# Kernel tuning notes

Hardware: AMD Instinct MI355X
Metric: run time of the kernel (lower is better)

The kernel has to match this reference:

```python
import jax, jax.numpy as jnp
import numpy as np

B, S, D, H = 4, 2048, 1024, 16
HD = D // H  # per-head dim = 64


def setup_inputs() -> dict:
    key = jax.random.key(0)
    ks = jax.random.split(key, 9)
    s = 1.0 / np.sqrt(HD)
    return {
        "query": jax.random.normal(ks[0], (B, S, D), jnp.float32),
        "key_": jax.random.normal(ks[1], (B, S, D), jnp.float32),
        "value": jax.random.normal(ks[2], (B, S, D), jnp.float32),
        "Wq": jax.random.uniform(ks[3], (HD, HD), jnp.float32, -s, s),
        "bq": jax.random.uniform(ks[4], (HD,), jnp.float32, -s, s),
        "Wk": jax.random.uniform(ks[5], (HD, HD), jnp.float32, -s, s),
        "bk": jax.random.uniform(ks[6], (HD,), jnp.float32, -s, s),
        "Wv": jax.random.uniform(ks[7], (HD, HD), jnp.float32, -s, s),
        "bv": jax.random.uniform(ks[8], (HD,), jnp.float32, -s, s),
    }


def _split_heads(x):
    # [B,S,D] -> [B,H,S,hd]
    return x.reshape(B, S, H, HD).transpose(0, 2, 1, 3)


def reference(query, key_, value, Wq, bq, Wk, bk, Wv, bv):
    q = _split_heads(query) @ Wq.T + bq  # [B,H,S,hd]
    k = _split_heads(key_) @ Wk.T + bk
    v = _split_heads(value) @ Wv.T + bv
    scores = jnp.einsum("bhqd,bhkd->bhqk", q, k) / jnp.sqrt(jnp.float32(HD))
    weights = jax.nn.softmax(scores, axis=-1)
    x_att = jnp.einsum("bhqk,bhkd->bhqd", weights, v)  # [B,H,S,hd]
    return x_att.transpose(0, 2, 1, 3).reshape(B, S, D)
```

## Files before the change

kernel.cpp:

```cpp
#include <hip/hip_runtime.h>
#include <hip/hip_bf16.h>


typedef float f32x4 __attribute__((ext_vector_type(4)));
typedef float f32x16 __attribute__((ext_vector_type(16)));
typedef __bf16 bf16x8 __attribute__((ext_vector_type(8)));
typedef unsigned short u16x4 __attribute__((ext_vector_type(4)));
typedef unsigned int u32x4 __attribute__((ext_vector_type(4)));

#define S_LEN 2048
#define D_MODEL 1024
#define HDIM 64
#define BH_TOT 64

static __device__ __forceinline__ unsigned short f2bf(float x) {
    __bf16 h = (__bf16)x;
    return __builtin_bit_cast(unsigned short, h);
}
static __device__ __forceinline__ unsigned int pk2(float lo, float hi) {
    return (unsigned int)f2bf(lo) | ((unsigned int)f2bf(hi) << 16);
}
static __device__ __forceinline__ bf16x8 cvt8(f32x4 a, f32x4 b) {
    bf16x8 r;
    #pragma unroll
    for (int j = 0; j < 4; ++j) { r[j] = (__bf16)a[j]; r[4 + j] = (__bf16)b[j]; }
    return r;
}

__global__ __launch_bounds__(256) void proj_kernel(
    const float* __restrict__ qin, const float* __restrict__ kin, const float* __restrict__ vin,
    const float* __restrict__ Wq, const float* __restrict__ bq,
    const float* __restrict__ Wk, const float* __restrict__ bk,
    const float* __restrict__ Wv, const float* __restrict__ bv,
    unsigned short* __restrict__ ws)
{
    const int bid = blockIdx.x;
    const int mat = bid >> 11;
    const int rem = bid & 2047;
    const int bh  = rem >> 5;
    const int st  = rem & 31;
    const int b = bh >> 4, h = bh & 15;

    const int tid = threadIdx.x;
    const int wave = tid >> 6, l = tid & 63;
    const int lr = l & 15, lg = l >> 4;

    const float* X    = (mat == 0) ? qin : (mat == 1) ? kin : vin;
    const float* W    = (mat == 0) ? Wq  : (mat == 1) ? Wk  : Wv;
    const float* bias = (mat == 0) ? bq  : (mat == 1) ? bk  : bv;

    const int s0 = st * 64 + wave * 16;

    bf16x8 af[2];
    {
        const size_t rowoff = ((size_t)(b * S_LEN + s0 + lr)) * D_MODEL + h * HDIM + lg * 8;
        #pragma unroll
        for (int kk = 0; kk < 2; ++kk) {
            const f32x4* p = (const f32x4*)(X + rowoff + kk * 32);
            af[kk] = cvt8(p[0], p[1]);
        }
    }
    bf16x8 wf[4][2];
    #pragma unroll
    for (int nt = 0; nt < 4; ++nt)
        #pragma unroll
        for (int kk = 0; kk < 2; ++kk) {
            const f32x4* p = (const f32x4*)(W + (nt * 16 + lr) * HDIM + kk * 32 + lg * 8);
            wf[nt][kk] = cvt8(p[0], p[1]);
        }

    unsigned short* qws  = ws;
    unsigned short* kws  = ws + (size_t)BH_TOT * S_LEN * HDIM;
    unsigned short* vtws = ws + 2 * (size_t)BH_TOT * S_LEN * HDIM;

    if (mat < 2) {
        f32x4 acc[4];
        #pragma unroll
        for (int nt = 0; nt < 4; ++nt)
            acc[nt] = *(const f32x4*)(bias + nt * 16 + lg * 4);
        #pragma unroll
        for (int nt = 0; nt < 4; ++nt)
            #pragma unroll
            for (int kk = 0; kk < 2; ++kk)
                acc[nt] = __builtin_amdgcn_mfma_f32_16x16x32_bf16(wf[nt][kk], af[kk], acc[nt], 0, 0, 0);

        const float sc = (mat == 0) ? 0.18033688011112042f : 1.0f;
        unsigned short* dst = (mat == 0) ? qws : kws;
        const size_t rowbase = ((size_t)bh * S_LEN + s0 + lr) * HDIM;
        #pragma unroll
        for (int nt = 0; nt < 4; ++nt) {
            u16x4 u;
            #pragma unroll
            for (int r = 0; r < 4; ++r) u[r] = f2bf(acc[nt][r] * sc);
            *(u16x4*)(dst + rowbase + nt * 16 + lg * 4) = u;
        }
    } else {
        f32x4 acc[4];
        #pragma unroll
        for (int nt = 0; nt < 4; ++nt) {
            float bb = bias[nt * 16 + lr];
            acc[nt][0] = bb; acc[nt][1] = bb; acc[nt][2] = bb; acc[nt][3] = bb;
        }
        #pragma unroll
        for (int nt = 0; nt < 4; ++nt)
            #pragma unroll
            for (int kk = 0; kk < 2; ++kk)
                acc[nt] = __builtin_amdgcn_mfma_f32_16x16x32_bf16(af[kk], wf[nt][kk], acc[nt], 0, 0, 0);
        #pragma unroll
        for (int nt = 0; nt < 4; ++nt) {
            u16x4 u;
            #pragma unroll
            for (int r = 0; r < 4; ++r) u[r] = f2bf(acc[nt][r]);
            *(u16x4*)(vtws + ((size_t)bh * HDIM + nt * 16 + lr) * S_LEN + s0 + lg * 4) = u;
        }
    }
}

__global__ __launch_bounds__(256, 3) void attn_kernel(
    const unsigned short* __restrict__ ws, float* __restrict__ out)
{
    const unsigned short* qws  = ws;
    const unsigned short* kws  = ws + (size_t)BH_TOT * S_LEN * HDIM;
    const unsigned short* vtws = ws + 2 * (size_t)BH_TOT * S_LEN * HDIM;

    __shared__ u32x4 ldsbuf[1024];
    char* ldsK = (char*)ldsbuf;
    char* ldsV = (char*)ldsbuf + 8192;

    const int bid = blockIdx.x;
    const int qt = bid & 15, bh = bid >> 4;
    const int b = bh >> 4, h = bh & 15;
    const int tid = threadIdx.x, wave = tid >> 6, l = tid & 63;
    const int q32 = l & 31, hi = l >> 5;

    const int qrow = qt * 128 + wave * 32 + q32;
    bf16x8 qf[4];
    {
        const unsigned short* qp = qws + ((size_t)bh * S_LEN + qrow) * HDIM + hi * 8;
        #pragma unroll
        for (int s = 0; s < 4; ++s) qf[s] = *(const bf16x8*)(qp + s * 16);
    }

    float m_run = -1e30f, l_run = 0.f;
    f32x16 oacc[2];
    #pragma unroll
    for (int i = 0; i < 16; ++i) { oacc[0][i] = 0.f; oacc[1][i] = 0.f; }

    const int srow = tid >> 3;
    const int scol = (tid & 7) * 16;
    const unsigned short* kbase = kws + (size_t)bh * S_LEN * HDIM;
    const unsigned short* vbase = vtws + (size_t)bh * HDIM * S_LEN;

    for (int t = 0; t < S_LEN / 64; ++t) {
        const int kv0 = t * 64;
        __syncthreads();
        #pragma unroll
        for (int p = 0; p < 2; ++p) {
            const int r = srow + p * 32;
            u32x4 val = *(const u32x4*)((const char*)(kbase + (size_t)(kv0 + r) * HDIM) + scol);
            *(u32x4*)(&ldsK[r * 128 + (scol ^ ((r & 7) << 4))]) = val;
        }
        #pragma unroll
        for (int p = 0; p < 2; ++p) {
            const int d = srow + p * 32;
            u32x4 val = *(const u32x4*)((const char*)(vbase + (size_t)d * S_LEN + kv0) + scol);
            *(u32x4*)(&ldsV[d * 128 + (scol ^ ((d & 7) << 4))]) = val;
        }
        __syncthreads();

        f32x16 sacc[2];
        #pragma unroll
        for (int i = 0; i < 16; ++i) { sacc[0][i] = 0.f; sacc[1][i] = 0.f; }
        #pragma unroll
        for (int m = 0; m < 2; ++m) {
            const int row = m * 32 + q32;
            const int swz = (row & 7) << 4;
            #pragma unroll
            for (int s = 0; s < 4; ++s) {
                bf16x8 kf = *(const bf16x8*)(&ldsK[row * 128 + ((s * 32 + hi * 16) ^ swz)]);
                sacc[m] = __builtin_amdgcn_mfma_f32_32x32x16_bf16(kf, qf[s], sacc[m], 0, 0, 0);
            }
        }

        float mx0 = sacc[0][0], mx1 = sacc[0][1], mx2 = sacc[0][2], mx3 = sacc[0][3];
        #pragma unroll
        for (int i = 4; i < 16; i += 4) {
            mx0 = fmaxf(mx0, sacc[0][i + 0]); mx1 = fmaxf(mx1, sacc[0][i + 1]);
            mx2 = fmaxf(mx2, sacc[0][i + 2]); mx3 = fmaxf(mx3, sacc[0][i + 3]);
        }
        #pragma unroll
        for (int i = 0; i < 16; i += 4) {
            mx0 = fmaxf(mx0, sacc[1][i + 0]); mx1 = fmaxf(mx1, sacc[1][i + 1]);
            mx2 = fmaxf(mx2, sacc[1][i + 2]); mx3 = fmaxf(mx3, sacc[1][i + 3]);
        }
        float pmax = fmaxf(fmaxf(mx0, mx1), fmaxf(mx2, mx3));
        pmax = fmaxf(pmax, __shfl_xor(pmax, 32));

        if (!__all(pmax <= m_run + 8.0f)) {
            const float mnew = fmaxf(m_run, pmax);
            const float fs = exp2f(m_run - mnew);
            m_run = mnew;
            l_run *= fs;
            #pragma unroll
            for (int reg = 0; reg < 16; ++reg) {
                const int qrw = (reg & 3) + 8 * (reg >> 2) + 4 * hi;
                const float fr = __shfl(fs, qrw);
                oacc[0][reg] *= fr; oacc[1][reg] *= fr;
            }
        }

        float s0a = 0.f, s1a = 0.f, s2a = 0.f, s3a = 0.f;
        #pragma unroll
        for (int m = 0; m < 2; ++m)
            #pragma unroll
            for (int i = 0; i < 16; i += 4) {
                float e0 = exp2f(sacc[m][i + 0] - m_run);
                float e1 = exp2f(sacc[m][i + 1] - m_run);
                float e2 = exp2f(sacc[m][i + 2] - m_run);
                float e3 = exp2f(sacc[m][i + 3] - m_run);
                sacc[m][i + 0] = e0; sacc[m][i + 1] = e1;
                sacc[m][i + 2] = e2; sacc[m][i + 3] = e3;
                s0a += e0; s1a += e1; s2a += e2; s3a += e3;
            }
        float rsum = (s0a + s1a) + (s2a + s3a);
        l_run += rsum + __shfl_xor(rsum, 32);

        bf16x8 pa[4];
        #pragma unroll
        for (int s = 0; s < 4; ++s) {
            const int m = s >> 1, rb = (s & 1) * 8;
            unsigned int c0 = pk2(sacc[m][rb + 0], sacc[m][rb + 1]);
            unsigned int c1 = pk2(sacc[m][rb + 2], sacc[m][rb + 3]);
            unsigned int c2 = pk2(sacc[m][rb + 4], sacc[m][rb + 5]);
            unsigned int c3 = pk2(sacc[m][rb + 6], sacc[m][rb + 7]);
            asm("v_permlane32_swap_b32 %0, %1" : "+v"(c0), "+v"(c2));
            asm("v_permlane32_swap_b32 %0, %1" : "+v"(c1), "+v"(c3));
            u32x4 packed = { c0, c1, c2, c3 };
            pa[s] = __builtin_bit_cast(bf16x8, packed);
        }

        #pragma unroll
        for (int dcol = 0; dcol < 2; ++dcol) {
            const int row = dcol * 32 + q32;
            const int swz = (row & 7) << 4;
            #pragma unroll
            for (int s = 0; s < 4; ++s) {
                bf16x8 vf = *(const bf16x8*)(&ldsV[row * 128 + ((s * 32 + hi * 16) ^ swz)]);
                oacc[dcol] = __builtin_amdgcn_mfma_f32_32x32x16_bf16(pa[s], vf, oacc[dcol], 0, 0, 0);
            }
        }
    }

    const float linv = 1.0f / l_run;
    float* obase = out + ((size_t)(b * S_LEN + qt * 128 + wave * 32)) * D_MODEL + h * HDIM;
    #pragma unroll
    for (int reg = 0; reg < 16; ++reg) {
        const int qrw = (reg & 3) + 8 * (reg >> 2) + 4 * hi;
        const float li = __shfl(linv, qrw);
        float* po = obase + (size_t)qrw * D_MODEL + q32;
        po[0]  = oacc[0][reg] * li;
        po[32] = oacc[1][reg] * li;
    }
}

extern "C" void kernel_launch(void* const* d_in, const int* in_sizes, int n_in,
                              void* d_out, int out_size, void* d_ws, size_t ws_size,
                              hipStream_t stream) {
    const float* qin = (const float*)d_in[0];
    const float* kin = (const float*)d_in[1];
    const float* vin = (const float*)d_in[2];
    const float* Wq  = (const float*)d_in[3];
    const float* bq  = (const float*)d_in[4];
    const float* Wk  = (const float*)d_in[5];
    const float* bk  = (const float*)d_in[6];
    const float* Wv  = (const float*)d_in[7];
    const float* bv  = (const float*)d_in[8];
    unsigned short* ws = (unsigned short*)d_ws;
    float* out = (float*)d_out;

    proj_kernel<<<dim3(3 * 2048), dim3(256), 0, stream>>>(qin, kin, vin, Wq, bq, Wk, bk, Wv, bv, ws);
    attn_kernel<<<dim3(1024), dim3(256), 0, stream>>>(ws, out);
}
```

Baseline: 312.5 us.

## Double-buffer K/V via direct global-to-LDS loads, split V projection with LDS transpose

The attention kernel now stages K and V tiles into double-buffered LDS using global_load_lds, prefetching the next tile while computing the current one. It also raises wave priority around the MFMA blocks and remaps block indices so heads group per XCD for L2 locality. The V projection moves into its own kernel that transposes through LDS so the transposed V is written with wide coalesced stores. The costs are twice the LDS per block, which may reduce occupancy, and one extra kernel launch.

```diff
diff --git a/kernel.cpp b/kernel.cpp
--- a/kernel.cpp
+++ b/kernel.cpp
@@ -26,12 +26,15 @@
     for (int j = 0; j < 4; ++j) { r[j] = (__bf16)a[j]; r[4 + j] = (__bf16)b[j]; }
     return r;
 }
-
-__global__ __launch_bounds__(256) void proj_kernel(
-    const float* __restrict__ qin, const float* __restrict__ kin, const float* __restrict__ vin,
+static __device__ __forceinline__ void gl_lds16(const void* g, void* l) {
+    __builtin_amdgcn_global_load_lds((const __attribute__((address_space(1))) void*)g,
+                                     (__attribute__((address_space(3))) void*)l, 16, 0, 0);
+}
+
+__global__ __launch_bounds__(256) void projqk_kernel(
+    const float* __restrict__ qin, const float* __restrict__ kin,
     const float* __restrict__ Wq, const float* __restrict__ bq,
     const float* __restrict__ Wk, const float* __restrict__ bk,
-    const float* __restrict__ Wv, const float* __restrict__ bv,
     unsigned short* __restrict__ ws)
 {
     const int bid = blockIdx.x;
@@ -45,9 +48,9 @@
     const int wave = tid >> 6, l = tid & 63;
     const int lr = l & 15, lg = l >> 4;
 
-    const float* X    = (mat == 0) ? qin : (mat == 1) ? kin : vin;
-    const float* W    = (mat == 0) ? Wq  : (mat == 1) ? Wk  : Wv;
-    const float* bias = (mat == 0) ? bq  : (mat == 1) ? bk  : bv;
+    const float* X    = (mat == 0) ? qin : kin;
+    const float* W    = (mat == 0) ? Wq  : Wk;
+    const float* bias = (mat == 0) ? bq  : bk;
 
     const int s0 = st * 64 + wave * 16;
 
@@ -69,51 +72,93 @@
             wf[nt][kk] = cvt8(p[0], p[1]);
         }
 
-    unsigned short* qws  = ws;
-    unsigned short* kws  = ws + (size_t)BH_TOT * S_LEN * HDIM;
+    f32x4 acc[4];
+    #pragma unroll
+    for (int nt = 0; nt < 4; ++nt)
+        acc[nt] = *(const f32x4*)(bias + nt * 16 + lg * 4);
+    #pragma unroll
+    for (int nt = 0; nt < 4; ++nt)
+        #pragma unroll
+        for (int kk = 0; kk < 2; ++kk)
+            acc[nt] = __builtin_amdgcn_mfma_f32_16x16x32_bf16(wf[nt][kk], af[kk], acc[nt], 0, 0, 0);
+
+    unsigned short* qws = ws;
+    unsigned short* kws = ws + (size_t)BH_TOT * S_LEN * HDIM;
+    const float sc = (mat == 0) ? 0.18033688011112042f : 1.0f;
+    unsigned short* dst = (mat == 0) ? qws : kws;
+    const size_t rowbase = ((size_t)bh * S_LEN + s0 + lr) * HDIM;
+    #pragma unroll
+    for (int nt = 0; nt < 4; ++nt) {
+        u16x4 u;
+        #pragma unroll
+        for (int r = 0; r < 4; ++r) u[r] = f2bf(acc[nt][r] * sc);
+        *(u16x4*)(dst + rowbase + nt * 16 + lg * 4) = u;
+    }
+}
+
+__global__ __launch_bounds__(256) void projv_kernel(
+    const float* __restrict__ vin,
+    const float* __restrict__ Wv, const float* __restrict__ bv,
+    unsigned short* __restrict__ ws)
+{
+    const int bid = blockIdx.x;
+    const int bh  = bid >> 5;
+    const int st  = bid & 31;
+    const int b = bh >> 4, h = bh & 15;
+
+    const int tid = threadIdx.x;
+    const int wave = tid >> 6, l = tid & 63;
+    const int lr = l & 15, lg = l >> 4;
+
+    __shared__ unsigned short T[64][72];
+
+    const int s0 = st * 64 + wave * 16;
+
+    bf16x8 af[2];
+    {
+        const size_t rowoff = ((size_t)(b * S_LEN + s0 + lr)) * D_MODEL + h * HDIM + lg * 8;
+        #pragma unroll
+        for (int kk = 0; kk < 2; ++kk) {
+            const f32x4* p = (const f32x4*)(vin + rowoff + kk * 32);
+            af[kk] = cvt8(p[0], p[1]);
+        }
+    }
+    bf16x8 wf[4][2];
+    #pragma unroll
+    for (int nt = 0; nt < 4; ++nt)
+        #pragma unroll
+        for (int kk = 0; kk < 2; ++kk) {
+            const f32x4* p = (const f32x4*)(Wv + (nt * 16 + lr) * HDIM + kk * 32 + lg * 8);
+            wf[nt][kk] = cvt8(p[0], p[1]);
+        }
+
+    f32x4 acc[4];
+    #pragma unroll
+    for (int nt = 0; nt < 4; ++nt) {
+        float bb = bv[nt * 16 + lr];
+        acc[nt][0] = bb; acc[nt][1] = bb; acc[nt][2] = bb; acc[nt][3] = bb;
+    }
+    #pragma unroll
+    for (int nt = 0; nt < 4; ++nt)
+        #pragma unroll
+        for (int kk = 0; kk < 2; ++kk)
+            acc[nt] = __builtin_amdgcn_mfma_f32_16x16x32_bf16(af[kk], wf[nt][kk], acc[nt], 0, 0, 0);
+
+    #pragma unroll
+    for (int nt = 0; nt < 4; ++nt) {
+        u16x4 u;
+        #pragma unroll
+        for (int r = 0; r < 4; ++r) u[r] = f2bf(acc[nt][r]);
+        *(u16x4*)&T[nt * 16 + lr][wave * 16 + lg * 4] = u;
+    }
+    __syncthreads();
+
     unsigned short* vtws = ws + 2 * (size_t)BH_TOT * S_LEN * HDIM;
-
-    if (mat < 2) {
-        f32x4 acc[4];
-        #pragma unroll
-        for (int nt = 0; nt < 4; ++nt)
-            acc[nt] = *(const f32x4*)(bias + nt * 16 + lg * 4);
-        #pragma unroll
-        for (int nt = 0; nt < 4; ++nt)
-            #pragma unroll
-            for (int kk = 0; kk < 2; ++kk)
-                acc[nt] = __builtin_amdgcn_mfma_f32_16x16x32_bf16(wf[nt][kk], af[kk], acc[nt], 0, 0, 0);
-
-        const float sc = (mat == 0) ? 0.18033688011112042f : 1.0f;
-        unsigned short* dst = (mat == 0) ? qws : kws;
-        const size_t rowbase = ((size_t)bh * S_LEN + s0 + lr) * HDIM;
-        #pragma unroll
-        for (int nt = 0; nt < 4; ++nt) {
-            u16x4 u;
-            #pragma unroll
-            for (int r = 0; r < 4; ++r) u[r] = f2bf(acc[nt][r] * sc);
-            *(u16x4*)(dst + rowbase + nt * 16 + lg * 4) = u;
-        }
-    } else {
-        f32x4 acc[4];
-        #pragma unroll
-        for (int nt = 0; nt < 4; ++nt) {
-            float bb = bias[nt * 16 + lr];
-            acc[nt][0] = bb; acc[nt][1] = bb; acc[nt][2] = bb; acc[nt][3] = bb;
-        }
-        #pragma unroll
-        for (int nt = 0; nt < 4; ++nt)
-            #pragma unroll
-            for (int kk = 0; kk < 2; ++kk)
-                acc[nt] = __builtin_amdgcn_mfma_f32_16x16x32_bf16(af[kk], wf[nt][kk], acc[nt], 0, 0, 0);
-        #pragma unroll
-        for (int nt = 0; nt < 4; ++nt) {
-            u16x4 u;
-            #pragma unroll
-            for (int r = 0; r < 4; ++r) u[r] = f2bf(acc[nt][r]);
-            *(u16x4*)(vtws + ((size_t)bh * HDIM + nt * 16 + lr) * S_LEN + s0 + lg * 4) = u;
-        }
-    }
+    const int d = tid >> 2, sc = (tid & 3) * 16;
+    const uint4* srcp = (const uint4*)&T[d][sc];
+    unsigned short* dstp = vtws + ((size_t)bh * HDIM + d) * S_LEN + st * 64 + sc;
+    ((uint4*)dstp)[0] = srcp[0];
+    ((uint4*)dstp)[1] = srcp[1];
 }
 
 __global__ __launch_bounds__(256, 3) void attn_kernel(
@@ -123,13 +168,15 @@
     const unsigned short* kws  = ws + (size_t)BH_TOT * S_LEN * HDIM;
     const unsigned short* vtws = ws + 2 * (size_t)BH_TOT * S_LEN * HDIM;
 
-    __shared__ u32x4 ldsbuf[1024];
-    char* ldsK = (char*)ldsbuf;
-    char* ldsV = (char*)ldsbuf + 8192;
+    __shared__ u32x4 ldsraw[2048];
+    char* ldsbuf = (char*)ldsraw;
 
     const int bid = blockIdx.x;
-    const int qt = bid & 15, bh = bid >> 4;
+    const int xcd = bid & 7, idx = bid >> 3;
+    const int qt = idx & 15;
+    const int bh = xcd + ((idx >> 4) << 3);
     const int b = bh >> 4, h = bh & 15;
+
     const int tid = threadIdx.x, wave = tid >> 6, l = tid & 63;
     const int q32 = l & 31, hi = l >> 5;
 
@@ -146,31 +193,44 @@
     #pragma unroll
     for (int i = 0; i < 16; ++i) { oacc[0][i] = 0.f; oacc[1][i] = 0.f; }
 
-    const int srow = tid >> 3;
-    const int scol = (tid & 7) * 16;
-    const unsigned short* kbase = kws + (size_t)bh * S_LEN * HDIM;
-    const unsigned short* vbase = vtws + (size_t)bh * HDIM * S_LEN;
+    const int lrow  = l >> 3;
+    const int lswz  = ((l & 7) * 16) ^ (lrow << 4);
+    const char* kgb = (const char*)(kws + (size_t)bh * S_LEN * HDIM);
+    const char* vgb = (const char*)(vtws + (size_t)bh * HDIM * S_LEN);
+
+    #define STAGE(bsel, kv0)                                                        \
+        do {                                                                        \
+            char* bK_ = ldsbuf + (bsel) * 16384;                                    \
+            char* bV_ = bK_ + 8192;                                                 \
+            _Pragma("unroll")                                                       \
+            for (int i_ = 0; i_ < 2; ++i_) {                                        \
+                const int r_ = wave * 16 + i_ * 8 + lrow;                           \
+                gl_lds16(kgb + (size_t)((kv0) + r_) * 128 + lswz,                   \
+                         bK_ + wave * 2048 + i_ * 1024);                            \
+                gl_lds16(vgb + (size_t)r_ * (S_LEN * 2) + (kv0) * 2 + lswz,         \
+                         bV_ + wave * 2048 + i_ * 1024);                            \
+            }                                                                       \
+        } while (0)
+
+    STAGE(0, 0);
+    int cur = 0;
 
     for (int t = 0; t < S_LEN / 64; ++t) {
-        const int kv0 = t * 64;
-        __syncthreads();
-        #pragma unroll
-        for (int p = 0; p < 2; ++p) {
-            const int r = srow + p * 32;
-            u32x4 val = *(const u32x4*)((const char*)(kbase + (size_t)(kv0 + r) * HDIM) + scol);
-            *(u32x4*)(&ldsK[r * 128 + (scol ^ ((r & 7) << 4))]) = val;
-        }
-        #pragma unroll
-        for (int p = 0; p < 2; ++p) {
-            const int d = srow + p * 32;
-            u32x4 val = *(const u32x4*)((const char*)(vbase + (size_t)d * S_LEN + kv0) + scol);
-            *(u32x4*)(&ldsV[d * 128 + (scol ^ ((d & 7) << 4))]) = val;
-        }
-        __syncthreads();
+        if (t < S_LEN / 64 - 1) {
+            STAGE(cur ^ 1, (t + 1) * 64);
+            asm volatile("s_waitcnt vmcnt(4)" ::: "memory");
+        } else {
+            asm volatile("s_waitcnt vmcnt(0)" ::: "memory");
+        }
+        __builtin_amdgcn_s_barrier();
+
+        const char* ldsK = ldsbuf + cur * 16384;
+        const char* ldsV = ldsK + 8192;
 
         f32x16 sacc[2];
         #pragma unroll
         for (int i = 0; i < 16; ++i) { sacc[0][i] = 0.f; sacc[1][i] = 0.f; }
+        __builtin_amdgcn_s_setprio(1);
         #pragma unroll
         for (int m = 0; m < 2; ++m) {
             const int row = m * 32 + q32;
@@ -181,6 +241,7 @@
                 sacc[m] = __builtin_amdgcn_mfma_f32_32x32x16_bf16(kf, qf[s], sacc[m], 0, 0, 0);
             }
         }
+        __builtin_amdgcn_s_setprio(0);
 
         float mx0 = sacc[0][0], mx1 = sacc[0][1], mx2 = sacc[0][2], mx3 = sacc[0][3];
         #pragma unroll
@@ -239,6 +300,7 @@
             pa[s] = __builtin_bit_cast(bf16x8, packed);
         }
 
+        __builtin_amdgcn_s_setprio(1);
         #pragma unroll
         for (int dcol = 0; dcol < 2; ++dcol) {
             const int row = dcol * 32 + q32;
@@ -249,7 +311,12 @@
                 oacc[dcol] = __builtin_amdgcn_mfma_f32_32x32x16_bf16(pa[s], vf, oacc[dcol], 0, 0, 0);
             }
         }
-    }
+        __builtin_amdgcn_s_setprio(0);
+
+        __builtin_amdgcn_s_barrier();
+        cur ^= 1;
+    }
+    #undef STAGE
 
     const float linv = 1.0f / l_run;
     float* obase = out + ((size_t)(b * S_LEN + qt * 128 + wave * 32)) * D_MODEL + h * HDIM;
@@ -278,6 +345,7 @@
     unsigned short* ws = (unsigned short*)d_ws;
     float* out = (float*)d_out;
 
-    proj_kernel<<<dim3(3 * 2048), dim3(256), 0, stream>>>(qin, kin, vin, Wq, bq, Wk, bk, Wv, bv, ws);
+    projqk_kernel<<<dim3(2 * 2048), dim3(256), 0, stream>>>(qin, kin, Wq, bq, Wk, bk, ws);
+    projv_kernel<<<dim3(2048), dim3(256), 0, stream>>>(vin, Wv, bv, ws);
     attn_kernel<<<dim3(1024), dim3(256), 0, stream>>>(ws, out);
 }
```

Result: faster. 301.8 us (-3.4%).
